# Kernel optimization log

Measured on AMD Instinct MI355X. Metric: run time of the kernel, lower is better.

The kernel has to match this reference:

```python
import jax, jax.numpy as jnp
import numpy as np
from jax import lax

B, N = 16, 2048
S0, S1, K = 256, 128, 32
EPS = 1e-5


def bn_relu(x, gamma, beta, axes):
    # training-mode BatchNorm (batch statistics) + ReLU; channel is last dim
    mean = jnp.mean(x, axis=axes, keepdims=True)
    var = jnp.var(x, axis=axes, keepdims=True)
    return jax.nn.relu((x - mean) * lax.rsqrt(var + EPS) * gamma + beta)


def fps(coords, s):
    # farthest point sampling, deterministic start at index 0. coords [B,N,3]
    b, n, _ = coords.shape
    def body(carry, _):
        dist, far = carry
        centroid = jnp.take_along_axis(coords, far[:, None, None], axis=1)  # [B,1,3]
        d = jnp.sum((coords - centroid) ** 2, axis=-1)                      # [B,N]
        dist = jnp.minimum(dist, d)
        return (dist, jnp.argmax(dist, axis=-1).astype(jnp.int32)), far
    init = (jnp.full((b, n), 1e10, coords.dtype), jnp.zeros((b,), jnp.int32))
    _, idx = lax.scan(body, init, None, length=s)
    return jnp.transpose(idx)  # [B,s]


def gather_points(pts, idx):
    # pts [B,N,C], idx [B,...] int -> [B,...,C]
    flat = idx.reshape(idx.shape[0], -1)[..., None]  # [B,M,1]
    out = jnp.take_along_axis(pts, flat, axis=1)     # [B,M,C]
    return out.reshape(*idx.shape, pts.shape[-1])


def sample_and_knn_group(s, k, coords, features):
    # coords [B,N,3], features [B,N,C] -> new_xyz [B,s,3], agg [B,s,k,2C]
    fps_idx = fps(coords, s)
    new_xyz = gather_points(coords, fps_idx)      # [B,s,3]
    center = gather_points(features, fps_idx)     # [B,s,C]
    d2 = jnp.sum((new_xyz[:, :, None, :] - coords[:, None, :, :]) ** 2, axis=-1)  # [B,s,N]
    _, knn_idx = lax.top_k(-d2, k)                # k smallest distances
    grouped = gather_points(features, knn_idx)    # [B,s,k,C]
    agg = jnp.concatenate(
        [grouped - center[:, :, None, :],
         jnp.broadcast_to(center[:, :, None, :], grouped.shape)], axis=-1)
    return new_xyz, agg


def sg_block(coords, features, s, k, w, gamma, beta):
    # conv1x1 -> BN -> ReLU -> max over k neighbors
    new_xyz, nf = sample_and_knn_group(s, k, coords, features)  # nf [B,s,k,d]
    h = jnp.einsum('bskd,od->bsko', nf, w)
    h = bn_relu(h, gamma, beta, axes=(0, 1, 2))
    return new_xyz, jnp.max(h, axis=2)  # [B,s,out]


def setup_inputs() -> dict:
    key = jax.random.key(0)
    ks = jax.random.split(key, 5)
    return {
        'x': jax.random.normal(ks[0], (B, 3, N), jnp.float32),
        'w1': jax.random.normal(ks[1], (64, 3), jnp.float32) * (1.0 / np.sqrt(3)),
        'g1': jnp.ones((64,), jnp.float32), 'b1': jnp.zeros((64,), jnp.float32),
        'w2': jax.random.normal(ks[2], (64, 64), jnp.float32) * 0.125,
        'g2': jnp.ones((64,), jnp.float32), 'b2': jnp.zeros((64,), jnp.float32),
        'w_sg0': jax.random.normal(ks[3], (128, 128), jnp.float32) * (1.0 / np.sqrt(128)),
        'g_sg0': jnp.ones((128,), jnp.float32), 'b_sg0': jnp.zeros((128,), jnp.float32),
        'w_sg1': jax.random.normal(ks[4], (256, 256), jnp.float32) * (1.0 / np.sqrt(256)),
        'g_sg1': jnp.ones((256,), jnp.float32), 'b_sg1': jnp.zeros((256,), jnp.float32),
    }


def reference(x, w1, g1, b1, w2, g2, b2, w_sg0, g_sg0, b_sg0, w_sg1, g_sg1, b_sg1):
    coords = jnp.transpose(x, (0, 2, 1))                   # [B,N,3]
    f = bn_relu(jnp.einsum('bnc,oc->bno', coords, w1), g1, b1, axes=(0, 1))  # [B,N,64]
    f = bn_relu(jnp.einsum('bnc,oc->bno', f, w2), g2, b2, axes=(0, 1))       # [B,N,64]
    xyz1, f1 = sg_block(coords, f, S0, K, w_sg0, g_sg0, b_sg0)   # [B,S0,128]
    _, f2 = sg_block(xyz1, f1, S1, K, w_sg1, g_sg1, b_sg1)       # [B,S1,256]
    return jnp.transpose(f2, (0, 2, 1))                           # [B,256,S1]
```

## Files before the change

### kernel.cpp

```cpp
#include <hip/hip_runtime.h>
#include <float.h>

#define BATCH 16
#define NPTS  2048
#define NS0   256
#define NS1   128
#define KK    32
#define EPSV  1e-5f
#define MROWS 32768.0f
#define M0F   131072.0f
#define M1F   65536.0f

__device__ __forceinline__ float sqdist(float ax,float ay,float az,float bx,float by,float bz){
  float dx=__fsub_rn(ax,bx), dy=__fsub_rn(ay,by), dz=__fsub_rn(az,bz);
  return __fadd_rn(__fadd_rn(__fmul_rn(dx,dx),__fmul_rn(dy,dy)),__fmul_rn(dz,dz));
}

template<int CTRL,int RM>
__device__ __forceinline__ float dpp_fmax_s(float x){
  int t = __builtin_amdgcn_update_dpp((int)0xFF800000, __float_as_int(x), CTRL, RM, 0xf, false);
  return fmaxf(x, __int_as_float(t));
}
template<int CTRL,int RM>
__device__ __forceinline__ float dpp_fmin_s(float x){
  int t = __builtin_amdgcn_update_dpp(0x7F800000, __float_as_int(x), CTRL, RM, 0xf, false);
  return fminf(x, __int_as_float(t));
}
template<int CTRL,int RM>
__device__ __forceinline__ unsigned dpp_umin_s(unsigned x){
  unsigned t = (unsigned)__builtin_amdgcn_update_dpp(-1, (int)x, CTRL, RM, 0xf, false);
  return t<x ? t : x;
}
__device__ __forceinline__ void wave_argmax_f32(float v, unsigned idx, float& mall, int& sel){
  float m=v;
  m=dpp_fmax_s<0x111,0xf>(m); m=dpp_fmax_s<0x112,0xf>(m); m=dpp_fmax_s<0x114,0xf>(m);
  m=dpp_fmax_s<0x118,0xf>(m); m=dpp_fmax_s<0x142,0xa>(m); m=dpp_fmax_s<0x143,0xc>(m);
  mall = __int_as_float(__builtin_amdgcn_readlane(__float_as_int(m),63));
  unsigned c = (v==mall)? idx : 0xFFFFFFFFu;
  c=dpp_umin_s<0x111,0xf>(c); c=dpp_umin_s<0x112,0xf>(c); c=dpp_umin_s<0x114,0xf>(c);
  c=dpp_umin_s<0x118,0xf>(c); c=dpp_umin_s<0x142,0xa>(c); c=dpp_umin_s<0x143,0xc>(c);
  sel = (int)(unsigned)__builtin_amdgcn_readlane((int)c,63);
}
__device__ __forceinline__ int wave_argmin_f32(float v, unsigned idx){
  float m=v;
  m=dpp_fmin_s<0x111,0xf>(m); m=dpp_fmin_s<0x112,0xf>(m); m=dpp_fmin_s<0x114,0xf>(m);
  m=dpp_fmin_s<0x118,0xf>(m); m=dpp_fmin_s<0x142,0xa>(m); m=dpp_fmin_s<0x143,0xc>(m);
  float mall = __int_as_float(__builtin_amdgcn_readlane(__float_as_int(m),63));
  unsigned c = (v==mall)? idx : 0xFFFFFFFFu;
  c=dpp_umin_s<0x111,0xf>(c); c=dpp_umin_s<0x112,0xf>(c); c=dpp_umin_s<0x114,0xf>(c);
  c=dpp_umin_s<0x118,0xf>(c); c=dpp_umin_s<0x142,0xa>(c); c=dpp_umin_s<0x143,0xc>(c);
  return (int)(unsigned)__builtin_amdgcn_readlane((int)c,63);
}


__device__ void embed1_body(int bid, const float* __restrict__ x, const float* __restrict__ w1,
                            float* __restrict__ coords, float* __restrict__ t1,
                            float* __restrict__ acc1S, float* __restrict__ acc1Q,
                            float* ls, float* lq){
  __shared__ float w[192];
  __shared__ float xs[3][64];
  __shared__ float fin[64][65];
  int tid = threadIdx.x;
  if (tid < 192) w[tid] = w1[tid];
  if (tid < 64){ ls[tid]=0.f; lq[tid]=0.f; }
  int base = bid*64;
  int b = base / NPTS, n0 = base % NPTS;
  if (tid < 192){
    int ch = tid>>6, i = tid&63;
    xs[ch][i] = x[((size_t)b*3+ch)*NPTS + n0 + i];
  }
  __syncthreads();
  if (tid < 64){
    coords[(size_t)(base+tid)*3+0]=xs[0][tid];
    coords[(size_t)(base+tid)*3+1]=xs[1][tid];
    coords[(size_t)(base+tid)*3+2]=xs[2][tid];
  }
  int p = tid>>2, c0 = (tid&3)<<4;
  float cx=xs[0][p], cy=xs[1][p], cz=xs[2][p];
  #pragma unroll
  for(int j=0;j<16;j++){
    int c = c0+j;
    fin[p][c] = cx*w[c*3+0] + cy*w[c*3+1] + cz*w[c*3+2];
  }
  __syncthreads();
  float s=0.f,q=0.f;
  for(int i=tid;i<4096;i+=256){
    int pp=i>>6, c=i&63;
    float v = fin[pp][c];
    t1[(size_t)base*64 + i] = v;
    s+=v; q+=v*v;
  }
  atomicAdd(&ls[tid&63], s);
  atomicAdd(&lq[tid&63], q);
  __syncthreads();
  if(tid<64){ atomicAdd(acc1S+tid, ls[tid]); atomicAdd(acc1Q+tid, lq[tid]); }
}

__device__ void wt_body(int gid, const float* __restrict__ w0, float* __restrict__ wt0,
                        const float* __restrict__ w1, float* __restrict__ wt1){
  if(gid < 128*128){
    int o = gid % 128, c = gid / 128;
    wt0[gid] = w0[o*128 + c];
  } else {
    int g2 = gid - 128*128;
    if(g2 >= 256*256) return;
    int o = g2 % 256, c = g2 / 256;
    wt1[g2] = w1[o*256 + c];
  }
}

__device__ void embed2_body(int bid, const float* __restrict__ t1, const float* __restrict__ w2,
                            const float* __restrict__ accS, const float* __restrict__ accQ,
                            const float* __restrict__ g1, const float* __restrict__ b1,
                            float* __restrict__ t2,
                            float* __restrict__ acc2S, float* __restrict__ acc2Q,
                            float* ls, float* lq, char* smem){
  float (*fin)[64] = (float(*)[64])smem;
  float* sm = (float*)smem + 4096;
  float* sr = sm+64; float* sg = sr+64; float* sb = sg+64;
  int tid = threadIdx.x;
  if (tid<64){
    float S=accS[tid], Q=accQ[tid];
    float m = S/MROWS, v = Q/MROWS - m*m; if(v<0.f) v=0.f;
    sm[tid]=m; sr[tid]=rsqrtf(v+EPSV); sg[tid]=g1[tid]; sb[tid]=b1[tid];
    ls[tid]=0.f; lq[tid]=0.f;
  }
  __syncthreads();
  int base = bid*64;
  for(int i=tid;i<4096;i+=256){
    int p=i>>6, c=i&63;
    float v = t1[(size_t)(base+p)*64 + c];
    v = (v - sm[c])*sr[c]*sg[c] + sb[c];
    fin[p][c] = v>0.f ? v : 0.f;
  }
  __syncthreads();
  int o = tid & 63, p0 = tid>>6;
  float acc[16];
  #pragma unroll
  for(int i=0;i<16;i++) acc[i]=0.f;
  for(int cc=0; cc<64; cc+=4){
    float4 wv = *(const float4*)(w2 + o*64 + cc);
    #pragma unroll
    for(int i=0;i<16;i++){
      float4 f4 = *(const float4*)&fin[p0 + i*4][cc];
      acc[i] += f4.x*wv.x + f4.y*wv.y + f4.z*wv.z + f4.w*wv.w;
    }
  }
  float s=0.f,q=0.f;
  #pragma unroll
  for(int i=0;i<16;i++){
    float v = acc[i];
    t2[(size_t)(base+p0+i*4)*64 + o] = v;
    s+=v; q+=v*v;
  }
  atomicAdd(&ls[o], s);
  atomicAdd(&lq[o], q);
  __syncthreads();
  if(tid<64){ atomicAdd(acc2S+tid, ls[tid]); atomicAdd(acc2Q+tid, lq[tid]); }
}

template<int P, int S, int T>
__device__ void fps_body(int b, const float* __restrict__ x, int* __restrict__ outIdx,
                         float* __restrict__ outXyz, char* smem){
  constexpr int PPT = P/T;
  constexpr int NW  = T/64;
  float* sx=(float*)smem; float* sy=sx+P; float* sz=sy+P;
  int* sidx=(int*)(sz+P);
  unsigned long long* rv64=(unsigned long long*)(sidx+S);
  int tid = threadIdx.x;
  const float* xb = x + (size_t)b*3*P;
  float px[PPT], py[PPT], pz[PPT], dist[PPT];
  #pragma unroll
  for(int i=0;i<PPT;i++){
    int n = i*T + tid;
    float X=xb[n], Y=xb[P+n], Z=xb[2*P+n];
    px[i]=X; py[i]=Y; pz[i]=Z; dist[i]=1e10f;
    sx[n]=X; sy[n]=Y; sz[n]=Z;
  }
  __syncthreads();
  int cur = 0;
  float cx=sx[0], cy=sy[0], cz=sz[0];
  for(int s=0;s<S;s++){
    if(tid==0) sidx[s]=cur;
    if(s==S-1) break;
    float bv=-FLT_MAX; int bi=0;
    #pragma unroll
    for(int i=0;i<PPT;i++){
      float d = sqdist(px[i],py[i],pz[i],cx,cy,cz);
      float nd = fminf(dist[i], d);
      dist[i]=nd;
      int n = i*T + tid;
      if(nd>bv){ bv=nd; bi=n; }
    }
    float mall; int sel;
    wave_argmax_f32(bv,(unsigned)bi,mall,sel);
    int sl = s & 1;
    if((tid&63)==0) rv64[sl*NW+(tid>>6)] = ((unsigned long long)__float_as_uint(mall)<<32)|(unsigned)(~sel);
    __syncthreads();
    unsigned long long wk = rv64[sl*NW];
    #pragma unroll
    for(int w=1;w<NW;w++){ unsigned long long t = rv64[sl*NW+w]; if(t>wk) wk=t; }
    cur = (int)(~(unsigned)wk);
    cx=sx[cur]; cy=sy[cur]; cz=sz[cur];
  }
  __syncthreads();
  for(int i=tid; i<S; i+=T){
    int id = sidx[i];
    outIdx[b*S+i] = id;
    outXyz[((size_t)b*S+i)*3+0] = sx[id];
    outXyz[((size_t)b*S+i)*3+1] = sy[id];
    outXyz[((size_t)b*S+i)*3+2] = sz[id];
  }
}

template<int P, int S>
__device__ void fps_wave_body(int b, const float* __restrict__ pts, int* __restrict__ outIdx,
                              float* __restrict__ outXyz, char* smem){
  constexpr int PPT = P/64;
  float4* sp = (float4*)smem;
  int* sidx = (int*)(smem + P*sizeof(float4));
  int lane = threadIdx.x;
  const float* p = pts + (size_t)b*P*3;
  float px[PPT], py[PPT], pz[PPT], dist[PPT];
  #pragma unroll
  for(int i=0;i<PPT;i++){
    int n = i*64 + lane;
    float X=p[n*3], Y=p[n*3+1], Z=p[n*3+2];
    px[i]=X; py[i]=Y; pz[i]=Z; dist[i]=1e10f;
    sp[n] = make_float4(X,Y,Z,0.f);
  }
  __syncthreads();
  int cur = 0;
  float cx=sp[0].x, cy=sp[0].y, cz=sp[0].z;
  for(int s=0;s<S;s++){
    if(lane==0) sidx[s]=cur;
    if(s==S-1) break;
    float bv=-FLT_MAX; int bi=0;
    #pragma unroll
    for(int i=0;i<PPT;i++){
      float d = sqdist(px[i],py[i],pz[i],cx,cy,cz);
      float nd = fminf(dist[i], d);
      dist[i]=nd;
      int n = i*64 + lane;
      if(nd>bv){ bv=nd; bi=n; }
    }
    float mall; int sel;
    wave_argmax_f32(bv,(unsigned)bi,mall,sel);
    cur = sel;
    float4 cp = sp[cur];
    cx=cp.x; cy=cp.y; cz=cp.z;
  }
  __syncthreads();
  for(int i=lane; i<S; i+=64){
    int id = sidx[i];
    float4 cp = sp[id];
    outIdx[b*S+i] = id;
    outXyz[((size_t)b*S+i)*3+0] = cp.x;
    outXyz[((size_t)b*S+i)*3+1] = cp.y;
    outXyz[((size_t)b*S+i)*3+2] = cp.z;
  }
}

template<int P>
__device__ void knn_body(int bq, const float* __restrict__ pts, const float* __restrict__ q,
                         int S, int* __restrict__ knn){
  constexpr int E = P/64;
  int lane = threadIdx.x;
  int b = bq / S;
  const float* p = pts + (size_t)b*P*3;
  float qx=q[(size_t)bq*3], qy=q[(size_t)bq*3+1], qz=q[(size_t)bq*3+2];
  float dl[E];
  float mv = FLT_MAX; unsigned mi = 0xFFFFFFFFu;
  #pragma unroll
  for(int i=0;i<E;i++){
    int n = i*64 + lane;
    float v = sqdist(qx,qy,qz,p[n*3],p[n*3+1],p[n*3+2]);
    dl[i] = v;
    if(v<mv){ mv=v; mi=(unsigned)n; }
  }
  for(int j=0;j<KK;j++){
    int sel = wave_argmin_f32(mv, mi);
    if(lane==0) knn[(size_t)bq*KK+j] = sel;
    if((sel & 63) == lane){
      int slot = sel >> 6;
      #pragma unroll
      for(int i=0;i<E;i++) if(i==slot) dl[i]=FLT_MAX;
      mv = FLT_MAX; mi = 0xFFFFFFFFu;
      #pragma unroll
      for(int i=0;i<E;i++){
        int n=i*64+lane;
        if(dl[i]<mv){ mv=dl[i]; mi=(unsigned)n; }
      }
    }
  }
}

template<int C, int P, int MODE>
__device__ void pass1_body(int bq, const float* __restrict__ feats, const float* __restrict__ feats2,
                           const int* __restrict__ knn,
                           const int* __restrict__ fpsIdx, const float* __restrict__ WT,
                           float* __restrict__ hmax, float* __restrict__ hmin,
                           float* __restrict__ part, int S,
                           const float* __restrict__ accS, const float* __restrict__ accQ,
                           const float* __restrict__ bg, const float* __restrict__ bb){
  constexpr int O   = 2*C;
  constexpr int TPB = C;
  constexpr int C4  = C/4;
  constexpr int OG  = O/8;
  constexpr int LDC = C+4;
  __shared__ __align__(16) float gfp[KK*LDC];
  __shared__ __align__(16) float cf[C];
  __shared__ __align__(16) float sa[C], sbb[C];
  __shared__ float sct[O];
  int tid = threadIdx.x;
  int b = bq / S;
  const float* fb = feats + (size_t)b*P*C;
  const float* fb2 = (MODE==2) ? feats2 + (size_t)b*P*C : nullptr;
  int ci = fpsIdx[bq];
  {
    float Mv = (MODE==1) ? MROWS : M0F;
    float S_=accS[tid], Q_=accQ[tid];
    float m = S_/Mv, vv = Q_/Mv - m*m; if(vv<0.f) vv=0.f;
    float a = rsqrtf(vv+EPSV)*bg[tid];
    float sh = bb[tid] - m*a;
    sa[tid]=a; sbb[tid]=sh;
    float raw;
    if(MODE==1) raw = fb[(size_t)ci*C + tid];
    else        raw = (a>=0.f) ? fb[(size_t)ci*C + tid] : fb2[(size_t)ci*C + tid];
    float cv = a*raw + sh;
    cf[tid] = cv>0.f ? cv : 0.f;
  }
  __syncthreads();
  for(int i=tid; i<KK*C4; i+=TPB){
    int k = i/C4, d4 = i - k*C4;
    size_t row = (size_t)knn[(size_t)bq*KK+k]*C;
    float4 a4 = *(const float4*)&sa[d4*4];
    float4 s4 = *(const float4*)&sbb[d4*4];
    float4 c4 = *(const float4*)&cf[d4*4];
    float4 g  = ((const float4*)(fb + row))[d4];
    float4 r;
    if(MODE==2){
      float4 g2 = ((const float4*)(fb2 + row))[d4];
      float gx = (a4.x>=0.f? g.x : g2.x)*a4.x + s4.x; gx = gx>0.f?gx:0.f;
      float gy = (a4.y>=0.f? g.y : g2.y)*a4.y + s4.y; gy = gy>0.f?gy:0.f;
      float gz = (a4.z>=0.f? g.z : g2.z)*a4.z + s4.z; gz = gz>0.f?gz:0.f;
      float gw = (a4.w>=0.f? g.w : g2.w)*a4.w + s4.w; gw = gw>0.f?gw:0.f;
      r.x=gx-c4.x; r.y=gy-c4.y; r.z=gz-c4.z; r.w=gw-c4.w;
    } else {
      float gx = a4.x*g.x+s4.x; gx = gx>0.f?gx:0.f;
      float gy = a4.y*g.y+s4.y; gy = gy>0.f?gy:0.f;
      float gz = a4.z*g.z+s4.z; gz = gz>0.f?gz:0.f;
      float gw = a4.w*g.w+s4.w; gw = gw>0.f?gw:0.f;
      r.x=gx-c4.x; r.y=gy-c4.y; r.z=gz-c4.z; r.w=gw-c4.w;
    }
    *(float4*)&gfp[k*LDC + d4*4] = r;
  }
  __syncthreads();
  {
    int o2 = tid*2;
    float ct0=0.f, ct1=0.f;
    for(int c=0;c<C;c+=4){
      float4 c4 = *(const float4*)&cf[c];
      #pragma unroll
      for(int t=0;t<4;t++){
        float cv = ((const float*)&c4)[t];
        float2 wh = *(const float2*)&WT[(size_t)(C+c+t)*O + o2];
        ct0 += cv*wh.x; ct1 += cv*wh.y;
      }
    }
    sct[o2]=ct0; sct[o2+1]=ct1;
  }
  __syncthreads();
  int kg = tid / OG;
  int og = tid % OG;
  float acc[8][8];
  #pragma unroll
  for(int a=0;a<8;a++)
    #pragma unroll
    for(int bb2=0;bb2<8;bb2++) acc[a][bb2]=0.f;
  for(int dc=0; dc<C4; dc++){
    float4 g4[8];
    #pragma unroll
    for(int jk=0;jk<8;jk++) g4[jk] = *(const float4*)&gfp[(kg*8+jk)*LDC + dc*4];
    #pragma unroll
    for(int t=0;t<4;t++){
      const float* wrow = WT + (size_t)(dc*4+t)*O + og*8;
      float4 wa = *(const float4*)wrow;
      float4 wb = *(const float4*)(wrow+4);
      #pragma unroll
      for(int jk=0;jk<8;jk++){
        float gs = ((const float*)&g4[jk])[t];
        acc[jk][0] += gs*wa.x; acc[jk][1] += gs*wa.y; acc[jk][2] += gs*wa.z; acc[jk][3] += gs*wa.w;
        acc[jk][4] += gs*wb.x; acc[jk][5] += gs*wb.y; acc[jk][6] += gs*wb.z; acc[jk][7] += gs*wb.w;
      }
    }
  }
  float tmx[8],tmn[8],tsm[8],tsq[8];
  #pragma unroll
  for(int jo=0;jo<8;jo++){
    int o = og*8+jo;
    float ct = sct[o];
    float s=0.f,q=0.f,mx=-FLT_MAX,mn=FLT_MAX;
    #pragma unroll
    for(int jk=0;jk<8;jk++){
      float h = acc[jk][jo] + ct;
      s+=h; q+=h*h; mx=fmaxf(mx,h); mn=fminf(mn,h);
    }
    tmx[jo]=mx; tmn[jo]=mn; tsm[jo]=s; tsq[jo]=q;
  }
  if constexpr (TPB==64){
    #pragma unroll
    for(int jo=0;jo<8;jo++){
      tmx[jo]=fmaxf(tmx[jo],__shfl_xor(tmx[jo],16)); tmx[jo]=fmaxf(tmx[jo],__shfl_xor(tmx[jo],32));
      tmn[jo]=fminf(tmn[jo],__shfl_xor(tmn[jo],16)); tmn[jo]=fminf(tmn[jo],__shfl_xor(tmn[jo],32));
      tsm[jo]+=__shfl_xor(tsm[jo],16); tsm[jo]+=__shfl_xor(tsm[jo],32);
      tsq[jo]+=__shfl_xor(tsq[jo],16); tsq[jo]+=__shfl_xor(tsq[jo],32);
    }
    if(tid<OG){
      #pragma unroll
      for(int jo=0;jo<8;jo++){
        int o = tid*8+jo;
        hmax[(size_t)bq*O+o]=tmx[jo]; hmin[(size_t)bq*O+o]=tmn[jo];
        part[(size_t)bq*2*O+o]=tsm[jo]; part[(size_t)bq*2*O+O+o]=tsq[jo];
      }
    }
  } else {
    #pragma unroll
    for(int jo=0;jo<8;jo++){
      tmx[jo]=fmaxf(tmx[jo],__shfl_xor(tmx[jo],32));
      tmn[jo]=fminf(tmn[jo],__shfl_xor(tmn[jo],32));
      tsm[jo]+=__shfl_xor(tsm[jo],32);
      tsq[jo]+=__shfl_xor(tsq[jo],32);
    }
    int wv = tid>>6;
    if((tid&63)<32){
      int og_ = tid&31;
      size_t rb = (size_t)bq*2 + wv;
      #pragma unroll
      for(int jo=0;jo<8;jo++){
        int o = og_*8+jo;
        hmax[rb*O+o]=tmx[jo]; hmin[rb*O+o]=tmn[jo];
        part[rb*2*O+o]=tsm[jo]; part[rb*2*O+O+o]=tsq[jo];
      }
    }
  }
}


__global__ __launch_bounds__(256) void k_embed1_wt(const float* __restrict__ x, const float* __restrict__ w1,
                         float* __restrict__ coords, float* __restrict__ t1,
                         const float* __restrict__ wsg0, float* __restrict__ wt0,
                         const float* __restrict__ wsg1, float* __restrict__ wt1,
                         float* __restrict__ acc1S, float* __restrict__ acc1Q){
  __shared__ float ls[64], lq[64];
  if(blockIdx.x < 512) embed1_body(blockIdx.x, x, w1, coords, t1, acc1S, acc1Q, ls, lq);
  else wt_body((blockIdx.x-512)*256 + threadIdx.x, wsg0, wt0, wsg1, wt1);
}

__global__ __launch_bounds__(256, 1) void k_fps0_embed2(const float* __restrict__ x,
                         int* __restrict__ fps0, float* __restrict__ xyz0,
                         const float* __restrict__ t1, const float* __restrict__ w2,
                         const float* __restrict__ acc1S, const float* __restrict__ acc1Q,
                         const float* __restrict__ g1, const float* __restrict__ b1,
                         float* __restrict__ t2,
                         float* __restrict__ acc2S, float* __restrict__ acc2Q){
  extern __shared__ char smem[];
  __shared__ float ls[64], lq[64];
  if(blockIdx.x < BATCH) fps_body<NPTS,NS0,256>(blockIdx.x, x, fps0, xyz0, smem);
  else embed2_body(blockIdx.x-BATCH, t1, w2, acc1S, acc1Q, g1, b1, t2, acc2S, acc2Q, ls, lq, smem);
}

__global__ __launch_bounds__(64, 4) void k_fps1_knn0(const float* __restrict__ xyz0,
                         int* __restrict__ fps1, float* __restrict__ xyz1,
                         const float* __restrict__ coords, int* __restrict__ knn0){
  extern __shared__ char smem[];
  if(blockIdx.x < BATCH) fps_wave_body<NS0,NS1>(blockIdx.x, xyz0, fps1, fps1 ? xyz1 : xyz1, smem);
  else knn_body<NPTS>(blockIdx.x-BATCH, coords, xyz0, NS0, knn0);
}

__global__ __launch_bounds__(64, 2) void k_pass1a_knn1(const float* __restrict__ t2,
                         const int* __restrict__ knn0, const int* __restrict__ fps0,
                         const float* __restrict__ wt0,
                         float* __restrict__ hmax0, float* __restrict__ hmin0, float* __restrict__ part0,
                         const float* __restrict__ acc2S, const float* __restrict__ acc2Q,
                         const float* __restrict__ g2, const float* __restrict__ b2,
                         const float* __restrict__ xyz0, const float* __restrict__ xyz1,
                         int* __restrict__ knn1){
  if(blockIdx.x < BATCH*NS0)
    pass1_body<64,NPTS,1>(blockIdx.x, t2, nullptr, knn0, fps0, wt0, hmax0, hmin0, part0, NS0,
                          acc2S, acc2Q, g2, b2);
  else
    knn_body<NS0>(blockIdx.x-BATCH*NS0, xyz0, xyz1, NS1, knn1);
}

__global__ __launch_bounds__(128, 2) void k_pass1b(const float* __restrict__ hmax0,
                         const float* __restrict__ hmin0,
                         const int* __restrict__ knn1, const int* __restrict__ fps1,
                         const float* __restrict__ wt1,
                         float* __restrict__ hmax1, float* __restrict__ hmin1, float* __restrict__ part1,
                         const float* __restrict__ accB0S, const float* __restrict__ accB0Q,
                         const float* __restrict__ gsg0, const float* __restrict__ bsg0){
  pass1_body<128,NS0,2>(blockIdx.x, hmax0, hmin0, knn1, fps1, wt1, hmax1, hmin1, part1, NS1,
                        accB0S, accB0Q, gsg0, bsg0);
}

__global__ __launch_bounds__(256) void k_statsB(const float* __restrict__ part, int W,
                                                float* __restrict__ acc){
  int tid = threadIdx.x;
  int r0 = blockIdx.x*64;
  for(int c=tid; c<W; c+=256){
    float a=0.f;
    for(int r=0;r<64;r++) a += part[(size_t)(r0+r)*W + c];
    atomicAdd(acc+c, a);
  }
}

__global__ __launch_bounds__(256) void k_post1tr(const float* __restrict__ hmax, const float* __restrict__ hmin,
        const float* __restrict__ aS, const float* __restrict__ aQ,
        const float* __restrict__ g, const float* __restrict__ bb, float* __restrict__ out){
  __shared__ float ssc[64], ssh[64];
  __shared__ float tile[64][129];
  int tid = threadIdx.x;
  int blk = blockIdx.x; int b = blk>>2; int c0 = (blk&3)*64;
  if(tid<64){
    int o = c0+tid;
    float m = aS[o]/M1F, v = aQ[o]/M1F - m*m; if(v<0.f) v=0.f;
    float sc = rsqrtf(v+EPSV)*g[o];
    ssc[tid]=sc; ssh[tid]=bb[o]-m*sc;
  }
  __syncthreads();
  for(int i=tid; i<128*64; i+=256){
    int r=i>>6, ch=i&63;
    size_t rb = (size_t)(b*NS1+r)*2;
    float sc = ssc[ch];
    float va = hmax[rb*256 + c0+ch], vb = hmax[(rb+1)*256 + c0+ch];
    float wa = hmin[rb*256 + c0+ch], wb = hmin[(rb+1)*256 + c0+ch];
    float h = (sc>=0.f) ? fmaxf(va,vb) : fminf(wa,wb);
    float v = h*sc + ssh[ch];
    tile[ch][r] = v>0.f ? v : 0.f;
  }
  __syncthreads();
  for(int i=tid; i<64*128; i+=256){
    int ch=i>>7, s=i&127;
    out[(size_t)b*(256*NS1) + (size_t)(c0+ch)*NS1 + s] = tile[ch][s];
  }
}

extern "C" void kernel_launch(void* const* d_in, const int* in_sizes, int n_in,
                              void* d_out, int out_size, void* d_ws, size_t ws_size,
                              hipStream_t stream){
  const float* x    = (const float*)d_in[0];
  const float* w1   = (const float*)d_in[1];
  const float* g1   = (const float*)d_in[2];
  const float* b1   = (const float*)d_in[3];
  const float* w2   = (const float*)d_in[4];
  const float* g2   = (const float*)d_in[5];
  const float* b2   = (const float*)d_in[6];
  const float* wsg0 = (const float*)d_in[7];
  const float* gsg0 = (const float*)d_in[8];
  const float* bsg0 = (const float*)d_in[9];
  const float* wsg1 = (const float*)d_in[10];
  const float* gsg1 = (const float*)d_in[11];
  const float* bsg1 = (const float*)d_in[12];
  float* out = (float*)d_out;

  float* wsf = (float*)d_ws;
  float* coords = wsf;                    wsf += BATCH*NPTS*3;
  float* t1     = wsf;                    wsf += BATCH*NPTS*64;
  float* t2     = wsf;                    wsf += BATCH*NPTS*64;
  float* acc1S=wsf; wsf+=64;  float* acc1Q=wsf; wsf+=64;
  float* acc2S=wsf; wsf+=64;  float* acc2Q=wsf; wsf+=64;
  float* accB0=wsf; wsf+=256;
  float* accB1=wsf; wsf+=512;
  int*   fps0 = (int*)wsf;                wsf += BATCH*NS0;
  float* xyz0 = wsf;                      wsf += BATCH*NS0*3;
  int*   knn0 = (int*)wsf;                wsf += BATCH*NS0*KK;
  float* hmax0= wsf;                      wsf += BATCH*NS0*128;
  float* hmin0= wsf;                      wsf += BATCH*NS0*128;
  float* part0= wsf;                      wsf += BATCH*NS0*2*128;
  int*   fps1 = (int*)wsf;                wsf += BATCH*NS1;
  float* xyz1 = wsf;                      wsf += BATCH*NS1*3;
  int*   knn1 = (int*)wsf;                wsf += BATCH*NS1*KK;
  float* wt0  = wsf;                      wsf += 128*128;
  float* wt1  = wsf;                      wsf += 256*256;
  float* part1 = t1;
  float* hmax1 = t2;
  float* hmin1 = t2 + BATCH*NS1*2*256;

  const int DYN_L3 = (NPTS*3 + NS0)*4 + 2*4*8;
  const int DYN_L4 = NS0*16 + NS1*4;

  hipMemsetAsync(acc1S, 0, 1024*sizeof(float), stream);
  k_embed1_wt<<<dim3(832), dim3(256), 0, stream>>>(x, w1, coords, t1, wsg0, wt0, wsg1, wt1,
                                                   acc1S, acc1Q);
  k_fps0_embed2<<<dim3(BATCH+512), dim3(256), DYN_L3, stream>>>(x, fps0, xyz0,
                                                  t1, w2, acc1S, acc1Q, g1, b1, t2, acc2S, acc2Q);
  k_fps1_knn0<<<dim3(BATCH + BATCH*NS0), dim3(64), DYN_L4, stream>>>(xyz0, fps1, xyz1, coords, knn0);
  k_pass1a_knn1<<<dim3(BATCH*NS0 + BATCH*NS1), dim3(64), 0, stream>>>(t2, knn0, fps0, wt0,
                                                  hmax0, hmin0, part0,
                                                  acc2S, acc2Q, g2, b2,
                                                  xyz0, xyz1, knn1);
  k_statsB<<<dim3(64), dim3(256), 0, stream>>>(part0, 256, accB0);
  k_pass1b<<<dim3(BATCH*NS1), dim3(128), 0, stream>>>(hmax0, hmin0, knn1, fps1, wt1,
                                                  hmax1, hmin1, part1,
                                                  accB0, accB0+128, gsg0, bsg0);
  k_statsB<<<dim3(64), dim3(256), 0, stream>>>(part1, 512, accB1);
  k_post1tr<<<dim3(64), dim3(256), 0, stream>>>(hmax1, hmin1, accB1, accB1+256, gsg1, bsg1, out);
}
```

Before: 416.2 us.

## Track top-two candidates in KNN selection and move embed1 stats to separate kernel

Each lane in the KNN selection now keeps its best and second-best distances, so that after its minimum is taken it can promote the second one. It only rescans its register array once both are used, using a bitmask of consumed slots. The memset is replaced by an extra block in the embed1 kernel that zeroes the accumulators. The per-block shared and global atomics for layer-1 statistics move into a new column-reduction kernel that rereads t1. This removes most rescans in the 32-step selection loop, but adds a kernel launch and an extra read of t1.

```diff
diff --git a/kernel.cpp b/kernel.cpp
--- a/kernel.cpp
+++ b/kernel.cpp
@@ -54,15 +54,12 @@
 
 
 __device__ void embed1_body(int bid, const float* __restrict__ x, const float* __restrict__ w1,
-                            float* __restrict__ coords, float* __restrict__ t1,
-                            float* __restrict__ acc1S, float* __restrict__ acc1Q,
-                            float* ls, float* lq){
+                            float* __restrict__ coords, float* __restrict__ t1){
   __shared__ float w[192];
   __shared__ float xs[3][64];
   __shared__ float fin[64][65];
   int tid = threadIdx.x;
   if (tid < 192) w[tid] = w1[tid];
-  if (tid < 64){ ls[tid]=0.f; lq[tid]=0.f; }
   int base = bid*64;
   int b = base / NPTS, n0 = base % NPTS;
   if (tid < 192){
@@ -83,17 +80,10 @@
     fin[p][c] = cx*w[c*3+0] + cy*w[c*3+1] + cz*w[c*3+2];
   }
   __syncthreads();
-  float s=0.f,q=0.f;
   for(int i=tid;i<4096;i+=256){
     int pp=i>>6, c=i&63;
-    float v = fin[pp][c];
-    t1[(size_t)base*64 + i] = v;
-    s+=v; q+=v*v;
-  }
-  atomicAdd(&ls[tid&63], s);
-  atomicAdd(&lq[tid&63], q);
-  __syncthreads();
-  if(tid<64){ atomicAdd(acc1S+tid, ls[tid]); atomicAdd(acc1Q+tid, lq[tid]); }
+    t1[(size_t)base*64 + i] = fin[pp][c];
+  }
 }
 
 __device__ void wt_body(int gid, const float* __restrict__ w0, float* __restrict__ wt0,
@@ -107,6 +97,19 @@
     int o = g2 % 256, c = g2 / 256;
     wt1[g2] = w1[o*256 + c];
   }
+}
+
+__device__ void statsA_body(int blk, const float* __restrict__ t,
+                            float* __restrict__ accS, float* __restrict__ accQ){
+  int c = threadIdx.x;
+  int r0 = blk*128;
+  float s=0.f, q=0.f;
+  for(int r=0;r<128;r++){
+    float v = t[(size_t)(r0+r)*64 + c];
+    s+=v; q+=v*v;
+  }
+  atomicAdd(accS+c, s);
+  atomicAdd(accQ+c, q);
 }
 
 __device__ void embed2_body(int bid, const float* __restrict__ t1, const float* __restrict__ w2,
@@ -270,26 +273,37 @@
   const float* p = pts + (size_t)b*P*3;
   float qx=q[(size_t)bq*3], qy=q[(size_t)bq*3+1], qz=q[(size_t)bq*3+2];
   float dl[E];
-  float mv = FLT_MAX; unsigned mi = 0xFFFFFFFFu;
+  float b1=FLT_MAX, b2=FLT_MAX;
+  unsigned i1=0xFFFFFFFFu, i2=0xFFFFFFFFu, consumed=0u;
   #pragma unroll
   for(int i=0;i<E;i++){
-    int n = i*64 + lane;
+    unsigned n = i*64 + lane;
     float v = sqdist(qx,qy,qz,p[n*3],p[n*3+1],p[n*3+2]);
     dl[i] = v;
-    if(v<mv){ mv=v; mi=(unsigned)n; }
+    bool lt1 = v<b1, lt2 = v<b2;
+    float    nb2 = lt1 ? b1 : (lt2 ? v : b2);
+    unsigned ni2 = lt1 ? i1 : (lt2 ? n : i2);
+    b1 = lt1 ? v : b1; i1 = lt1 ? n : i1;
+    b2 = nb2; i2 = ni2;
   }
   for(int j=0;j<KK;j++){
-    int sel = wave_argmin_f32(mv, mi);
+    int sel = wave_argmin_f32(b1, i1);
     if(lane==0) knn[(size_t)bq*KK+j] = sel;
     if((sel & 63) == lane){
-      int slot = sel >> 6;
-      #pragma unroll
-      for(int i=0;i<E;i++) if(i==slot) dl[i]=FLT_MAX;
-      mv = FLT_MAX; mi = 0xFFFFFFFFu;
-      #pragma unroll
-      for(int i=0;i<E;i++){
-        int n=i*64+lane;
-        if(dl[i]<mv){ mv=dl[i]; mi=(unsigned)n; }
+      consumed |= 1u << (sel >> 6);
+      b1 = b2; i1 = i2;
+      b2 = FLT_MAX; i2 = 0xFFFFFFFFu;
+      if(b1 == FLT_MAX){
+        #pragma unroll
+        for(int i=0;i<E;i++){
+          float v = ((consumed>>i)&1u) ? FLT_MAX : dl[i];
+          unsigned n = i*64 + lane;
+          bool lt1 = v<b1, lt2 = v<b2;
+          float    nb2 = lt1 ? b1 : (lt2 ? v : b2);
+          unsigned ni2 = lt1 ? i1 : (lt2 ? n : i2);
+          b1 = lt1 ? v : b1; i1 = lt1 ? n : i1;
+          b2 = nb2; i2 = ni2;
+        }
       }
     }
   }
@@ -451,10 +465,18 @@
                          float* __restrict__ coords, float* __restrict__ t1,
                          const float* __restrict__ wsg0, float* __restrict__ wt0,
                          const float* __restrict__ wsg1, float* __restrict__ wt1,
-                         float* __restrict__ acc1S, float* __restrict__ acc1Q){
-  __shared__ float ls[64], lq[64];
-  if(blockIdx.x < 512) embed1_body(blockIdx.x, x, w1, coords, t1, acc1S, acc1Q, ls, lq);
-  else wt_body((blockIdx.x-512)*256 + threadIdx.x, wsg0, wt0, wsg1, wt1);
+                         float* __restrict__ accz){
+  if(blockIdx.x < 512) embed1_body(blockIdx.x, x, w1, coords, t1);
+  else if(blockIdx.x < 832) wt_body((blockIdx.x-512)*256 + threadIdx.x, wsg0, wt0, wsg1, wt1);
+  else {
+    int tid = threadIdx.x;
+    accz[tid]=0.f; accz[tid+256]=0.f; accz[tid+512]=0.f; accz[tid+768]=0.f;
+  }
+}
+
+__global__ __launch_bounds__(64) void k_statsA(const float* __restrict__ t,
+                         float* __restrict__ accS, float* __restrict__ accQ){
+  statsA_body(blockIdx.x, t, accS, accQ);
 }
 
 __global__ __launch_bounds__(256, 1) void k_fps0_embed2(const float* __restrict__ x,
@@ -474,7 +496,7 @@
                          int* __restrict__ fps1, float* __restrict__ xyz1,
                          const float* __restrict__ coords, int* __restrict__ knn0){
   extern __shared__ char smem[];
-  if(blockIdx.x < BATCH) fps_wave_body<NS0,NS1>(blockIdx.x, xyz0, fps1, fps1 ? xyz1 : xyz1, smem);
+  if(blockIdx.x < BATCH) fps_wave_body<NS0,NS1>(blockIdx.x, xyz0, fps1, xyz1, smem);
   else knn_body<NPTS>(blockIdx.x-BATCH, coords, xyz0, NS0, knn0);
 }
 
@@ -590,9 +612,8 @@
   const int DYN_L3 = (NPTS*3 + NS0)*4 + 2*4*8;
   const int DYN_L4 = NS0*16 + NS1*4;
 
-  hipMemsetAsync(acc1S, 0, 1024*sizeof(float), stream);
-  k_embed1_wt<<<dim3(832), dim3(256), 0, stream>>>(x, w1, coords, t1, wsg0, wt0, wsg1, wt1,
-                                                   acc1S, acc1Q);
+  k_embed1_wt<<<dim3(833), dim3(256), 0, stream>>>(x, w1, coords, t1, wsg0, wt0, wsg1, wt1, acc1S);
+  k_statsA<<<dim3(256), dim3(64), 0, stream>>>(t1, acc1S, acc1Q);
   k_fps0_embed2<<<dim3(BATCH+512), dim3(256), DYN_L3, stream>>>(x, fps0, xyz0,
                                                   t1, w2, acc1S, acc1Q, g1, b1, t2, acc2S, acc2Q);
   k_fps1_knn0<<<dim3(BATCH + BATCH*NS0), dim3(64), DYN_L4, stream>>>(xyz0, fps1, xyz1, coords, knn0);
```

Result: faster. 402.4 us (-3.3%).
